# Performance work log

Measured on AMD Instinct MI355X. Metric: run time of the kernel, lower is better.

## Reference

```python
import jax, jax.numpy as jnp
import numpy as np

B, V = 1024, 16            # batch, n_variables
NH, SHARE = 32, 4          # n_base_heads, n_heads_sharing_slider
SH = NH // SHARE           # n_slider_heads = 8
D = 128                    # n_token_dim
KV = D * SH                # kv_size = 1024
H = 4096                   # n_hidden


def setup_inputs() -> dict:
    key = jax.random.key(0)
    ks = jax.random.split(key, 14)
    s = 0.02
    inp = {
        "prefix": jax.random.uniform(ks[0], (B, V), jnp.float32, -1.0, 1.0),
        # stacked per-variable key-encoder weights
        "kW1": jax.random.normal(ks[1], (V, KV), jnp.float32) * s,
        "kb1": jnp.zeros((V, KV), jnp.float32),
        "kW2": jax.random.normal(ks[2], (V, KV, H), jnp.float32) * s,
        "kb2": jnp.zeros((V, H), jnp.float32),
        "kW3": jax.random.normal(ks[3], (V, H, KV), jnp.float32) * s,
        "kb3": jnp.zeros((V, KV), jnp.float32),
        # stacked per-variable value-encoder weights
        "vW1": jax.random.normal(ks[4], (V, KV), jnp.float32) * s,
        "vb1": jnp.zeros((V, KV), jnp.float32),
        "vW2": jax.random.normal(ks[5], (V, KV, H), jnp.float32) * s,
        "vb2": jnp.zeros((V, H), jnp.float32),
        "vW3": jax.random.normal(ks[6], (V, H, KV), jnp.float32) * s,
        "vb3": jnp.zeros((V, KV), jnp.float32),
        "attention_factor": jnp.zeros((), jnp.float32),
    }
    return inp


def _mlp(x, W1, b1, W2, b2, W3, b3):
    # x: [B, V] scalar slider per variable; stacked tiny MLPs over V.
    h = jnp.tanh(x[:, :, None] * W1[None] + b1[None])            # [B,V,KV]
    h = jnp.tanh(jnp.einsum('bvk,vkh->bvh', h, W2) + b2[None])   # [B,V,H]
    return jnp.einsum('bvh,vhk->bvk', h, W3) + b3[None]          # [B,V,KV]


def _to_heads(x):
    # [B,V,KV] -> [B, n_base_heads, V, D] with repeat_interleave over slider heads
    x = x.reshape(B, V, SH, D)
    x = jnp.repeat(x, SHARE, axis=2)            # [B,V,NH,D]
    return jnp.transpose(x, (0, 2, 1, 3))       # [B,NH,V,D]


def reference(prefix, kW1, kb1, kW2, kb2, kW3, kb3,
              vW1, vb1, vW2, vb2, vW3, vb3, attention_factor):
    keys = _to_heads(_mlp(prefix, kW1, kb1, kW2, kb2, kW3, kb3))
    values = _to_heads(_mlp(prefix, vW1, vb1, vW2, vb2, vW3, vb3))
    return keys, values, attention_factor
```

## Files before the change

### kernel.cpp

```cpp
#include <hip/hip_runtime.h>
#include <hip/hip_bf16.h>
#include <cstdint>

#define B_   1024
#define V_   16
#define NH_  32
#define SH_  8
#define D_   128
#define KV_  1024
#define H_   4096

typedef __bf16 bf16;
typedef bf16  bf16x8 __attribute__((ext_vector_type(8)));
typedef float f32x2  __attribute__((ext_vector_type(2)));
typedef float f32x4  __attribute__((ext_vector_type(4)));

#define VMCNT(n) asm volatile("s_waitcnt vmcnt(" #n ")" ::: "memory")
#define LGKM0()  asm volatile("s_waitcnt lgkmcnt(0)" ::: "memory")

__device__ __forceinline__ void gl2lds16(const void* g, void* l) {
    __builtin_amdgcn_global_load_lds((const __attribute__((address_space(1))) void*)g,
                                     (__attribute__((address_space(3))) void*)l,
                                     16, 0, 0);
}

__global__ __launch_bounds__(256)
void h1_kernel(const float* __restrict__ prefix,
               const float* __restrict__ W1a, const float* __restrict__ b1a,
               const float* __restrict__ W1b, const float* __restrict__ b1b,
               bf16* __restrict__ h1)
{
    int gid = blockIdx.x * 256 + threadIdx.x;
    int k8  = gid & 127;
    int b   = (gid >> 7) & 1023;
    int vm  = gid >> 17;
    int v   = vm & 15;
    const float* W1 = (vm >> 4) ? W1b : W1a;
    const float* b1 = (vm >> 4) ? b1b : b1a;
    float x = prefix[b * V_ + v];
    const float* wp = W1 + (size_t)v * KV_ + k8 * 8;
    const float* bp = b1 + (size_t)v * KV_ + k8 * 8;
    f32x4 w0 = *(const f32x4*)wp,       w1 = *(const f32x4*)(wp + 4);
    f32x4 q0 = *(const f32x4*)bp,       q1 = *(const f32x4*)(bp + 4);
    bf16x8 o;
#pragma unroll
    for (int j = 0; j < 4; ++j) o[j]     = (bf16)tanhf(fmaf(x, w0[j], q0[j]));
#pragma unroll
    for (int j = 0; j < 4; ++j) o[4 + j] = (bf16)tanhf(fmaf(x, w1[j], q1[j]));
    *(bf16x8*)(h1 + (size_t)gid * 8) = o;
}

template<int MODE, int KDIM, int NDIM>
__global__ __launch_bounds__(512)
void gemm_t2(const bf16* __restrict__ A0, const bf16* __restrict__ A1,
             const float* __restrict__ Bf0, const float* __restrict__ Bf1,
             const float* __restrict__ bias0, const float* __restrict__ bias1,
             bf16* __restrict__ outB0, bf16* __restrict__ outB1,
             float* __restrict__ outF)
{
    __shared__ __align__(16) char smem[131072];

    constexpr int NX  = NDIM / 256;
    constexpr int NMB = 4;
    constexpr int NXY = NX * NMB;
    const int lin = blockIdx.x + NX * blockIdx.y + NXY * blockIdx.z;
    constexpr int NWG = NXY * 32;
    constexpr int CHK = NWG / 8;
    const int swz = (lin & 7) * CHK + (lin >> 3);
    const int mm  = swz / (NXY * 16);
    const int r2  = swz - mm * (NXY * 16);
    const int v   = r2 / NXY;
    const int rem = r2 - v * NXY;
    const int m0  = (rem / NX) * 256;
    const int n0  = (rem - (rem / NX) * NX) * 256;

    const bf16*  Abase = mm ? A1 : A0;
    const float* Bbase = mm ? Bf1 : Bf0;
    const float* bias  = mm ? bias1 : bias0;

    const int t  = threadIdx.x;
    const int l  = t & 63;
    const int w  = t >> 6;
    const int wr = w >> 2;
    const int wc = w & 3;
    constexpr int NT = KDIM / 64;
    static_assert(NT >= 4, "NT >= 4");

    const bf16*  Av = Abase + (size_t)v * 1024 * KDIM + (size_t)m0 * KDIM;
    const float* Bv = Bbase + (size_t)v * KDIM * NDIM + n0;

    f32x4 acc[8][4];
#pragma unroll
    for (int i = 0; i < 8; ++i)
#pragma unroll
        for (int j = 0; j < 4; ++j) acc[i][j] = f32x4{0.f, 0.f, 0.f, 0.f};

    const float* bptr = Bv + (size_t)((t >> 7) * 16) * NDIM + 2 * (t & 127);
    f32x2 br[16];

    auto loadBR = [&](int ktile) {
        const float* np = bptr + (size_t)ktile * 64 * NDIM;
#pragma unroll
        for (int j = 0; j < 16; ++j) br[j] = *(const f32x2*)(np + (size_t)j * NDIM);
    };
    auto stageA = [&](int ktile, int ab) {
#pragma unroll
        for (int i = 0; i < 4; ++i) {
            const int off = t + i * 512;
            const int row = off >> 3;
            const int gc  = (off & 7) ^ ((row >> 1) & 7);
            gl2lds16(Av + (size_t)row * KDIM + ktile * 64 + gc * 8,
                     smem + (size_t)ab * 32768 + (size_t)off * 16);
        }
    };
    auto writeB = [&](int bb) {
        bf16* bN = (bf16*)(smem + 65536 + (size_t)bb * 32768);
#pragma unroll
        for (int i = 0; i < 2; ++i)
#pragma unroll
            for (int h = 0; h < 2; ++h) {
                bf16x8 pk;
#pragma unroll
                for (int jj = 0; jj < 8; ++jj) pk[jj] = (bf16)br[h * 8 + jj][i];
                const int n  = 2 * (t & 127) + i;
                const int ch = ((t >> 7) * 2 + h) ^ (t & 7);
                *(bf16x8*)(bN + (size_t)n * 64 + ch * 8) = pk;
            }
    };
    auto mfmaStep = [&](int kt) {
        const bf16* aC = (const bf16*)(smem + (size_t)(kt & 1) * 32768);
        const bf16* bC = (const bf16*)(smem + 65536 + (size_t)(kt & 1) * 32768);
#pragma unroll
        for (int kk = 0; kk < 2; ++kk) {
            bf16x8 af[8], bfv[4];
#pragma unroll
            for (int f = 0; f < 8; ++f) {
                const int mr = wr * 128 + f * 16 + (l & 15);
                const int ca = (kk * 4 + (l >> 4)) ^ ((mr >> 1) & 7);
                af[f] = *(const bf16x8*)(aC + (size_t)mr * 64 + ca * 8);
            }
#pragma unroll
            for (int f = 0; f < 4; ++f) {
                const int nr = wc * 64 + f * 16 + (l & 15);
                const int cb = (kk * 4 + (l >> 4)) ^ ((nr >> 1) & 7);
                bfv[f] = *(const bf16x8*)(bC + (size_t)nr * 64 + cb * 8);
            }
#pragma unroll
            for (int fm = 0; fm < 8; ++fm)
#pragma unroll
                for (int fn = 0; fn < 4; ++fn)
                    acc[fm][fn] = __builtin_amdgcn_mfma_f32_16x16x32_bf16(
                        af[fm], bfv[fn], acc[fm][fn], 0, 0, 0);
        }
    };

    loadBR(0);
    stageA(0, 0);
    VMCNT(4);
    writeB(0);
    VMCNT(0);
    LGKM0();
    __builtin_amdgcn_s_barrier();

    for (int kt = 0; kt < NT - 1; ++kt) {
        loadBR(kt + 1);
        stageA(kt + 1, (kt + 1) & 1);
        mfmaStep(kt);
        VMCNT(4);
        writeB((kt + 1) & 1);
        VMCNT(0);
        LGKM0();
        __builtin_amdgcn_s_barrier();
    }
    mfmaStep(NT - 1);

    const int rbase = (l >> 4) * 4;
    const int cbase = l & 15;
    if (MODE == 0) {
        bf16* outB = mm ? outB1 : outB0;
        __syncthreads();
        bf16* scr = (bf16*)(smem + (size_t)w * 16384);
#pragma unroll
        for (int fn = 0; fn < 4; ++fn) {
            const int c  = fn * 16 + cbase;
            const float bv = bias[(size_t)v * NDIM + n0 + wc * 64 + c];
#pragma unroll
            for (int fm = 0; fm < 8; ++fm)
#pragma unroll
                for (int j = 0; j < 4; ++j) {
                    const int r = fm * 16 + rbase + j;
                    scr[r * 64 + (c ^ (((r >> 2) & 3) << 4))] =
                        (bf16)tanhf(acc[fm][fn][j] + bv);
                }
        }
        const int c8 = (l & 7) * 8;
#pragma unroll
        for (int i = 0; i < 16; ++i) {
            const int r  = i * 8 + (l >> 3);
            bf16x8 val = *(const bf16x8*)&scr[r * 64 + (c8 ^ (((r >> 2) & 3) << 4))];
            const int mr = m0 + wr * 128 + r;
            const int nc = n0 + wc * 64 + c8;
            __builtin_nontemporal_store(val,
                (bf16x8*)(outB + (size_t)v * 1024 * NDIM + (size_t)mr * NDIM + nc));
        }
    } else {
        float* outm = outF + (size_t)mm * ((size_t)B_ * NH_ * V_ * D_);
        __syncthreads();
        float* scr = (float*)(smem + (size_t)w * 16384);
        const int nb = n0 + wc * 64;
        const int sh = nb >> 7;
        const int db = nb & 127;
#pragma unroll
        for (int p = 0; p < 2; ++p) {
#pragma unroll
            for (int fm = 0; fm < 8; ++fm)
#pragma unroll
                for (int fq = 0; fq < 2; ++fq) {
                    const int fn = 2 * p + fq;
#pragma unroll
                    for (int j = 0; j < 4; ++j) {
                        const int r = fm * 16 + rbase + j;
                        const int c = fq * 16 + cbase;
                        scr[r * 32 + (c ^ (((r >> 2) & 1) << 4))] = acc[fm][fn][j];
                    }
                }
            const int c4   = (l & 7) * 4;
            const int colg = p * 32 + c4;
            f32x4 bv4;
#pragma unroll
            for (int q = 0; q < 4; ++q)
                bv4[q] = bias[(size_t)v * NDIM + nb + colg + q];
#pragma unroll
            for (int i = 0; i < 16; ++i) {
                const int r = i * 8 + (l >> 3);
                f32x4 val = *(const f32x4*)&scr[r * 32 + (c4 ^ (((r >> 2) & 1) << 4))];
#pragma unroll
                for (int q = 0; q < 4; ++q) val[q] += bv4[q];
                const int mr = m0 + wr * 128 + r;
                float* pp = outm + (size_t)mr * (NH_ * V_ * D_)
                                 + (size_t)(sh * 4) * (V_ * D_)
                                 + (size_t)v * D_ + db + colg;
                __builtin_nontemporal_store(val, (f32x4*)(pp));
                __builtin_nontemporal_store(val, (f32x4*)(pp + V_ * D_));
                __builtin_nontemporal_store(val, (f32x4*)(pp + 2 * V_ * D_));
                __builtin_nontemporal_store(val, (f32x4*)(pp + 3 * V_ * D_));
            }
        }
    }
}

__global__ void tail_kernel(const float* __restrict__ af, float* __restrict__ out)
{
    out[0] = af[0];
}

extern "C" void kernel_launch(void* const* d_in, const int* in_sizes, int n_in,
                              void* d_out, int out_size, void* d_ws, size_t ws_size,
                              hipStream_t stream)
{
    const float* prefix = (const float*)d_in[0];
    const float* W1[2]  = {(const float*)d_in[1], (const float*)d_in[7]};
    const float* b1[2]  = {(const float*)d_in[2], (const float*)d_in[8]};
    const float* W2[2]  = {(const float*)d_in[3], (const float*)d_in[9]};
    const float* b2[2]  = {(const float*)d_in[4], (const float*)d_in[10]};
    const float* W3[2]  = {(const float*)d_in[5], (const float*)d_in[11]};
    const float* b3[2]  = {(const float*)d_in[6], (const float*)d_in[12]};
    const float* afac   = (const float*)d_in[13];

    bf16* h1  = (bf16*)d_ws;
    bf16* h2a = (bf16*)((char*)d_ws + (size_t)67108864);
    bf16* h2b = (bf16*)((char*)d_ws + (size_t)67108864 + (size_t)134217728);
    float* outp = (float*)d_out;

    h1_kernel<<<16384, 256, 0, stream>>>(prefix, W1[0], b1[0], W1[1], b1[1], h1);
    gemm_t2<0, 1024, 4096><<<dim3(16, 4, 32), 512, 0, stream>>>(
        h1, h1 + (size_t)16777216, W2[0], W2[1], b2[0], b2[1],
        h2a, h2b, nullptr);
    gemm_t2<1, 4096, 1024><<<dim3(4, 4, 32), 512, 0, stream>>>(
        h2a, h2b, W3[0], W3[1], b3[0], b3[1],
        nullptr, nullptr, outp);
    tail_kernel<<<1, 1, 0, stream>>>(afac, outp + (size_t)2 * B_ * NH_ * V_ * D_);
}
```

Before: 868.0 us.

## Prefetch B weights two k-tiles ahead with double register banks and MFMA priority

The B-operand (fp32 weight) register prefetch becomes two k-tiles deep, using two alternating register banks with adjusted vmcnt waits, so global-load latency is hidden behind more MFMA work. The MFMA section is wrapped in s_setprio to favour math issue, and launch bounds request 2 blocks per CU. The extra 32 registers per thread plus the 2-block launch bound may cause spills or lower occupancy, since the 128KB shared memory already limits residency.

```diff
diff --git a/kernel.cpp b/kernel.cpp
--- a/kernel.cpp
+++ b/kernel.cpp
@@ -51,8 +51,8 @@
 }
 
 template<int MODE, int KDIM, int NDIM>
-__global__ __launch_bounds__(512)
-void gemm_t2(const bf16* __restrict__ A0, const bf16* __restrict__ A1,
+__global__ __launch_bounds__(512, 2)
+void gemm_t4(const bf16* __restrict__ A0, const bf16* __restrict__ A1,
              const float* __restrict__ Bf0, const float* __restrict__ Bf1,
              const float* __restrict__ bias0, const float* __restrict__ bias1,
              bf16* __restrict__ outB0, bf16* __restrict__ outB1,
@@ -84,7 +84,7 @@
     const int wr = w >> 2;
     const int wc = w & 3;
     constexpr int NT = KDIM / 64;
-    static_assert(NT >= 4, "NT >= 4");
+    static_assert(NT >= 4 && (NT % 2) == 0, "NT even, >= 4");
 
     const bf16*  Av = Abase + (size_t)v * 1024 * KDIM + (size_t)m0 * KDIM;
     const float* Bv = Bbase + (size_t)v * KDIM * NDIM + n0;
@@ -96,12 +96,12 @@
         for (int j = 0; j < 4; ++j) acc[i][j] = f32x4{0.f, 0.f, 0.f, 0.f};
 
     const float* bptr = Bv + (size_t)((t >> 7) * 16) * NDIM + 2 * (t & 127);
-    f32x2 br[16];
-
-    auto loadBR = [&](int ktile) {
+    f32x2 brA[16], brB[16];
+
+    auto loadBR = [&](int ktile, f32x2 (&bank)[16]) {
         const float* np = bptr + (size_t)ktile * 64 * NDIM;
 #pragma unroll
-        for (int j = 0; j < 16; ++j) br[j] = *(const f32x2*)(np + (size_t)j * NDIM);
+        for (int j = 0; j < 16; ++j) bank[j] = *(const f32x2*)(np + (size_t)j * NDIM);
     };
     auto stageA = [&](int ktile, int ab) {
 #pragma unroll
@@ -113,7 +113,7 @@
                      smem + (size_t)ab * 32768 + (size_t)off * 16);
         }
     };
-    auto writeB = [&](int bb) {
+    auto writeB = [&](f32x2 (&bank)[16], int bb) {
         bf16* bN = (bf16*)(smem + 65536 + (size_t)bb * 32768);
 #pragma unroll
         for (int i = 0; i < 2; ++i)
@@ -121,7 +121,7 @@
             for (int h = 0; h < 2; ++h) {
                 bf16x8 pk;
 #pragma unroll
-                for (int jj = 0; jj < 8; ++jj) pk[jj] = (bf16)br[h * 8 + jj][i];
+                for (int jj = 0; jj < 8; ++jj) pk[jj] = (bf16)bank[h * 8 + jj][i];
                 const int n  = 2 * (t & 127) + i;
                 const int ch = ((t >> 7) * 2 + h) ^ (t & 7);
                 *(bf16x8*)(bN + (size_t)n * 64 + ch * 8) = pk;
@@ -130,6 +130,7 @@
     auto mfmaStep = [&](int kt) {
         const bf16* aC = (const bf16*)(smem + (size_t)(kt & 1) * 32768);
         const bf16* bC = (const bf16*)(smem + 65536 + (size_t)(kt & 1) * 32768);
+        __builtin_amdgcn_s_setprio(1);
 #pragma unroll
         for (int kk = 0; kk < 2; ++kk) {
             bf16x8 af[8], bfv[4];
@@ -152,22 +153,37 @@
                     acc[fm][fn] = __builtin_amdgcn_mfma_f32_16x16x32_bf16(
                         af[fm], bfv[fn], acc[fm][fn], 0, 0, 0);
         }
-    };
-
-    loadBR(0);
+        __builtin_amdgcn_s_setprio(0);
+    };
+
+    loadBR(0, brA);
     stageA(0, 0);
-    VMCNT(4);
-    writeB(0);
-    VMCNT(0);
+    loadBR(1, brB);
+    VMCNT(20);
+    writeB(brA, 0);
+    VMCNT(16);
     LGKM0();
     __builtin_amdgcn_s_barrier();
 
-    for (int kt = 0; kt < NT - 1; ++kt) {
-        loadBR(kt + 1);
+    auto stepS = [&](int kt, f32x2 (&brIss)[16], f32x2 (&brUse)[16]) {
         stageA(kt + 1, (kt + 1) & 1);
+        loadBR(kt + 2, brIss);
         mfmaStep(kt);
+        VMCNT(20);
+        writeB(brUse, (kt + 1) & 1);
+        VMCNT(16);
+        LGKM0();
+        __builtin_amdgcn_s_barrier();
+    };
+    for (int kt = 0; kt + 3 < NT; kt += 2) {
+        stepS(kt,     brA, brB);
+        stepS(kt + 1, brB, brA);
+    }
+    {
+        stageA(NT - 1, (NT - 1) & 1);
+        mfmaStep(NT - 2);
         VMCNT(4);
-        writeB((kt + 1) & 1);
+        writeB(brB, (NT - 1) & 1);
         VMCNT(0);
         LGKM0();
         __builtin_amdgcn_s_barrier();
@@ -273,10 +289,10 @@
     float* outp = (float*)d_out;
 
     h1_kernel<<<16384, 256, 0, stream>>>(prefix, W1[0], b1[0], W1[1], b1[1], h1);
-    gemm_t2<0, 1024, 4096><<<dim3(16, 4, 32), 512, 0, stream>>>(
+    gemm_t4<0, 1024, 4096><<<dim3(16, 4, 32), 512, 0, stream>>>(
         h1, h1 + (size_t)16777216, W2[0], W2[1], b2[0], b2[1],
         h2a, h2b, nullptr);
-    gemm_t2<1, 4096, 1024><<<dim3(4, 4, 32), 512, 0, stream>>>(
+    gemm_t4<1, 4096, 1024><<<dim3(4, 4, 32), 512, 0, stream>>>(
         h2a, h2b, W3[0], W3[1], b3[0], b3[1],
         nullptr, nullptr, outp);
     tail_kernel<<<1, 1, 0, stream>>>(afac, outp + (size_t)2 * B_ * NH_ * V_ * D_);
```

After: 2.339 ms. 2.69x slower.

## Fuse first-layer tanh activation into the first GEMM's A-tile producer

Applied to the files above, without the earlier changes.

Removes the separate h1 kernel and its 64MB bf16 intermediate buffer. The first GEMM now loads W1, b1 and the prefix slice into LDS and computes the tanh(x*W1+b1) A tiles on the fly for each k-tile, instead of streaming A from global memory. This trades global memory traffic for recomputed tanh work. Each A tile is recomputed once per N-block (16 times) and adds extra LDS use, which could reduce occupancy.

```diff
diff --git a/kernel.cpp b/kernel.cpp
--- a/kernel.cpp
+++ b/kernel.cpp
@@ -24,41 +24,19 @@
                                      16, 0, 0);
 }
 
-__global__ __launch_bounds__(256)
-void h1_kernel(const float* __restrict__ prefix,
-               const float* __restrict__ W1a, const float* __restrict__ b1a,
-               const float* __restrict__ W1b, const float* __restrict__ b1b,
-               bf16* __restrict__ h1)
-{
-    int gid = blockIdx.x * 256 + threadIdx.x;
-    int k8  = gid & 127;
-    int b   = (gid >> 7) & 1023;
-    int vm  = gid >> 17;
-    int v   = vm & 15;
-    const float* W1 = (vm >> 4) ? W1b : W1a;
-    const float* b1 = (vm >> 4) ? b1b : b1a;
-    float x = prefix[b * V_ + v];
-    const float* wp = W1 + (size_t)v * KV_ + k8 * 8;
-    const float* bp = b1 + (size_t)v * KV_ + k8 * 8;
-    f32x4 w0 = *(const f32x4*)wp,       w1 = *(const f32x4*)(wp + 4);
-    f32x4 q0 = *(const f32x4*)bp,       q1 = *(const f32x4*)(bp + 4);
-    bf16x8 o;
-#pragma unroll
-    for (int j = 0; j < 4; ++j) o[j]     = (bf16)tanhf(fmaf(x, w0[j], q0[j]));
-#pragma unroll
-    for (int j = 0; j < 4; ++j) o[4 + j] = (bf16)tanhf(fmaf(x, w1[j], q1[j]));
-    *(bf16x8*)(h1 + (size_t)gid * 8) = o;
-}
-
-template<int MODE, int KDIM, int NDIM>
 __global__ __launch_bounds__(512)
-void gemm_t2(const bf16* __restrict__ A0, const bf16* __restrict__ A1,
+void gemm1_f(const float* __restrict__ prefix,
+             const float* __restrict__ W1a, const float* __restrict__ b1a,
+             const float* __restrict__ W1b, const float* __restrict__ b1b,
              const float* __restrict__ Bf0, const float* __restrict__ Bf1,
              const float* __restrict__ bias0, const float* __restrict__ bias1,
-             bf16* __restrict__ outB0, bf16* __restrict__ outB1,
-             float* __restrict__ outF)
+             bf16* __restrict__ outB0, bf16* __restrict__ outB1)
 {
-    __shared__ __align__(16) char smem[131072];
+    constexpr int KDIM = 1024, NDIM = 4096;
+    __shared__ __align__(16) char smem[140288];
+    float* w1L = (float*)(smem + 131072);
+    float* b1L = (float*)(smem + 135168);
+    float* pfL = (float*)(smem + 139264);
 
     constexpr int NX  = NDIM / 256;
     constexpr int NMB = 4;
@@ -74,9 +52,11 @@
     const int m0  = (rem / NX) * 256;
     const int n0  = (rem - (rem / NX) * NX) * 256;
 
-    const bf16*  Abase = mm ? A1 : A0;
-    const float* Bbase = mm ? Bf1 : Bf0;
-    const float* bias  = mm ? bias1 : bias0;
+    const float* W1v = (mm ? W1b : W1a) + (size_t)v * KV_;
+    const float* b1v = (mm ? b1b : b1a) + (size_t)v * KV_;
+    const float* Bv  = (mm ? Bf1 : Bf0) + (size_t)v * KDIM * NDIM + n0;
+    const float* bias = mm ? bias1 : bias0;
+    bf16* outB = mm ? outB1 : outB0;
 
     const int t  = threadIdx.x;
     const int l  = t & 63;
@@ -84,7 +64,169 @@
     const int wr = w >> 2;
     const int wc = w & 3;
     constexpr int NT = KDIM / 64;
-    static_assert(NT >= 4, "NT >= 4");
+
+    f32x4 acc[8][4];
+#pragma unroll
+    for (int i = 0; i < 8; ++i)
+#pragma unroll
+        for (int j = 0; j < 4; ++j) acc[i][j] = f32x4{0.f, 0.f, 0.f, 0.f};
+
+    const float* bptr = Bv + (size_t)((t >> 7) * 16) * NDIM + 2 * (t & 127);
+    f32x2 br[16];
+
+    auto loadBR = [&](int ktile) {
+        const float* np = bptr + (size_t)ktile * 64 * NDIM;
+#pragma unroll
+        for (int j = 0; j < 16; ++j) br[j] = *(const f32x2*)(np + (size_t)j * NDIM);
+    };
+    auto computeA = [&](int ktile, int ab) {
+#pragma unroll
+        for (int i = 0; i < 4; ++i) {
+            const int off = t + i * 512;
+            const int row = off >> 3;
+            const int gc  = (off & 7) ^ ((row >> 1) & 7);
+            const int kb  = ktile * 64 + gc * 8;
+            const float x = pfL[row];
+            f32x4 wa = *(const f32x4*)&w1L[kb],     wb = *(const f32x4*)&w1L[kb + 4];
+            f32x4 qa = *(const f32x4*)&b1L[kb],     qb = *(const f32x4*)&b1L[kb + 4];
+            bf16x8 o;
+#pragma unroll
+            for (int j = 0; j < 4; ++j) o[j]     = (bf16)tanhf(fmaf(x, wa[j], qa[j]));
+#pragma unroll
+            for (int j = 0; j < 4; ++j) o[4 + j] = (bf16)tanhf(fmaf(x, wb[j], qb[j]));
+            *(bf16x8*)(smem + (size_t)ab * 32768 + (size_t)off * 16) = o;
+        }
+    };
+    auto writeB = [&](int bb) {
+        bf16* bN = (bf16*)(smem + 65536 + (size_t)bb * 32768);
+#pragma unroll
+        for (int i = 0; i < 2; ++i)
+#pragma unroll
+            for (int h = 0; h < 2; ++h) {
+                bf16x8 pk;
+#pragma unroll
+                for (int jj = 0; jj < 8; ++jj) pk[jj] = (bf16)br[h * 8 + jj][i];
+                const int n  = 2 * (t & 127) + i;
+                const int ch = ((t >> 7) * 2 + h) ^ (t & 7);
+                *(bf16x8*)(bN + (size_t)n * 64 + ch * 8) = pk;
+            }
+    };
+    auto mfmaStep = [&](int kt) {
+        const bf16* aC = (const bf16*)(smem + (size_t)(kt & 1) * 32768);
+        const bf16* bC = (const bf16*)(smem + 65536 + (size_t)(kt & 1) * 32768);
+#pragma unroll
+        for (int kk = 0; kk < 2; ++kk) {
+            bf16x8 af[8], bfv[4];
+#pragma unroll
+            for (int f = 0; f < 8; ++f) {
+                const int mr = wr * 128 + f * 16 + (l & 15);
+                const int ca = (kk * 4 + (l >> 4)) ^ ((mr >> 1) & 7);
+                af[f] = *(const bf16x8*)(aC + (size_t)mr * 64 + ca * 8);
+            }
+#pragma unroll
+            for (int f = 0; f < 4; ++f) {
+                const int nr = wc * 64 + f * 16 + (l & 15);
+                const int cb = (kk * 4 + (l >> 4)) ^ ((nr >> 1) & 7);
+                bfv[f] = *(const bf16x8*)(bC + (size_t)nr * 64 + cb * 8);
+            }
+#pragma unroll
+            for (int fm = 0; fm < 8; ++fm)
+#pragma unroll
+                for (int fn = 0; fn < 4; ++fn)
+                    acc[fm][fn] = __builtin_amdgcn_mfma_f32_16x16x32_bf16(
+                        af[fm], bfv[fn], acc[fm][fn], 0, 0, 0);
+        }
+    };
+
+    loadBR(0);
+    if (t < 256) {
+        f32x4 wv = *(const f32x4*)(W1v + t * 4);
+        float pf = prefix[(size_t)(m0 + t) * V_ + v];
+        *(f32x4*)&w1L[t * 4] = wv;
+        pfL[t] = pf;
+    } else {
+        f32x4 qv = *(const f32x4*)(b1v + (t - 256) * 4);
+        *(f32x4*)&b1L[(t - 256) * 4] = qv;
+    }
+    __syncthreads();
+    computeA(0, 0);
+    writeB(0);
+    LGKM0();
+    __builtin_amdgcn_s_barrier();
+
+    for (int kt = 0; kt < NT - 1; ++kt) {
+        loadBR(kt + 1);
+        computeA(kt + 1, (kt + 1) & 1);
+        mfmaStep(kt);
+        VMCNT(0);
+        writeB((kt + 1) & 1);
+        LGKM0();
+        __builtin_amdgcn_s_barrier();
+    }
+    mfmaStep(NT - 1);
+
+    const int rbase = (l >> 4) * 4;
+    const int cbase = l & 15;
+    __syncthreads();
+    bf16* scr = (bf16*)(smem + (size_t)w * 16384);
+#pragma unroll
+    for (int fn = 0; fn < 4; ++fn) {
+        const int c  = fn * 16 + cbase;
+        const float bv = bias[(size_t)v * NDIM + n0 + wc * 64 + c];
+#pragma unroll
+        for (int fm = 0; fm < 8; ++fm)
+#pragma unroll
+            for (int j = 0; j < 4; ++j) {
+                const int r = fm * 16 + rbase + j;
+                scr[r * 64 + (c ^ (((r >> 2) & 3) << 4))] =
+                    (bf16)tanhf(acc[fm][fn][j] + bv);
+            }
+    }
+    const int c8 = (l & 7) * 8;
+#pragma unroll
+    for (int i = 0; i < 16; ++i) {
+        const int r  = i * 8 + (l >> 3);
+        bf16x8 val = *(const bf16x8*)&scr[r * 64 + (c8 ^ (((r >> 2) & 3) << 4))];
+        const int mr = m0 + wr * 128 + r;
+        const int nc = n0 + wc * 64 + c8;
+        __builtin_nontemporal_store(val,
+            (bf16x8*)(outB + (size_t)v * 1024 * NDIM + (size_t)mr * NDIM + nc));
+    }
+}
+
+__global__ __launch_bounds__(512)
+void gemm2_k(const bf16* __restrict__ A0, const bf16* __restrict__ A1,
+             const float* __restrict__ Bf0, const float* __restrict__ Bf1,
+             const float* __restrict__ bias0, const float* __restrict__ bias1,
+             float* __restrict__ outF)
+{
+    constexpr int KDIM = 4096, NDIM = 1024;
+    __shared__ __align__(16) char smem[131072];
+
+    constexpr int NX  = NDIM / 256;
+    constexpr int NMB = 4;
+    constexpr int NXY = NX * NMB;
+    const int lin = blockIdx.x + NX * blockIdx.y + NXY * blockIdx.z;
+    constexpr int NWG = NXY * 32;
+    constexpr int CHK = NWG / 8;
+    const int swz = (lin & 7) * CHK + (lin >> 3);
+    const int mm  = swz / (NXY * 16);
+    const int r2  = swz - mm * (NXY * 16);
+    const int v   = r2 / NXY;
+    const int rem = r2 - v * NXY;
+    const int m0  = (rem / NX) * 256;
+    const int n0  = (rem - (rem / NX) * NX) * 256;
+
+    const bf16*  Abase = mm ? A1 : A0;
+    const float* Bbase = mm ? Bf1 : Bf0;
+    const float* bias  = mm ? bias1 : bias0;
+
+    const int t  = threadIdx.x;
+    const int l  = t & 63;
+    const int w  = t >> 6;
+    const int wr = w >> 2;
+    const int wc = w & 3;
+    constexpr int NT = KDIM / 64;
 
     const bf16*  Av = Abase + (size_t)v * 1024 * KDIM + (size_t)m0 * KDIM;
     const float* Bv = Bbase + (size_t)v * KDIM * NDIM + n0;
@@ -176,75 +318,46 @@
 
     const int rbase = (l >> 4) * 4;
     const int cbase = l & 15;
-    if (MODE == 0) {
-        bf16* outB = mm ? outB1 : outB0;
-        __syncthreads();
-        bf16* scr = (bf16*)(smem + (size_t)w * 16384);
-#pragma unroll
-        for (int fn = 0; fn < 4; ++fn) {
-            const int c  = fn * 16 + cbase;
-            const float bv = bias[(size_t)v * NDIM + n0 + wc * 64 + c];
-#pragma unroll
-            for (int fm = 0; fm < 8; ++fm)
+    float* outm = outF + (size_t)mm * ((size_t)B_ * NH_ * V_ * D_);
+    __syncthreads();
+    float* scr = (float*)(smem + (size_t)w * 16384);
+    const int nb = n0 + wc * 64;
+    const int sh = nb >> 7;
+    const int db = nb & 127;
+#pragma unroll
+    for (int p = 0; p < 2; ++p) {
+#pragma unroll
+        for (int fm = 0; fm < 8; ++fm)
+#pragma unroll
+            for (int fq = 0; fq < 2; ++fq) {
+                const int fn = 2 * p + fq;
 #pragma unroll
                 for (int j = 0; j < 4; ++j) {
                     const int r = fm * 16 + rbase + j;
-                    scr[r * 64 + (c ^ (((r >> 2) & 3) << 4))] =
-                        (bf16)tanhf(acc[fm][fn][j] + bv);
+                    const int c = fq * 16 + cbase;
+                    scr[r * 32 + (c ^ (((r >> 2) & 1) << 4))] = acc[fm][fn][j];
                 }
-        }
-        const int c8 = (l & 7) * 8;
+            }
+        const int c4   = (l & 7) * 4;
+        const int colg = p * 32 + c4;
+        f32x4 bv4;
+#pragma unroll
+        for (int q = 0; q < 4; ++q)
+            bv4[q] = bias[(size_t)v * NDIM + nb + colg + q];
 #pragma unroll
         for (int i = 0; i < 16; ++i) {
-            const int r  = i * 8 + (l >> 3);
-            bf16x8 val = *(const bf16x8*)&scr[r * 64 + (c8 ^ (((r >> 2) & 3) << 4))];
+            const int r = i * 8 + (l >> 3);
+            f32x4 val = *(const f32x4*)&scr[r * 32 + (c4 ^ (((r >> 2) & 1) << 4))];
+#pragma unroll
+            for (int q = 0; q < 4; ++q) val[q] += bv4[q];
             const int mr = m0 + wr * 128 + r;
-            const int nc = n0 + wc * 64 + c8;
-            __builtin_nontemporal_store(val,
-                (bf16x8*)(outB + (size_t)v * 1024 * NDIM + (size_t)mr * NDIM + nc));
-        }
-    } else {
-        float* outm = outF + (size_t)mm * ((size_t)B_ * NH_ * V_ * D_);
-        __syncthreads();
-        float* scr = (float*)(smem + (size_t)w * 16384);
-        const int nb = n0 + wc * 64;
-        const int sh = nb >> 7;
-        const int db = nb & 127;
-#pragma unroll
-        for (int p = 0; p < 2; ++p) {
-#pragma unroll
-            for (int fm = 0; fm < 8; ++fm)
-#pragma unroll
-                for (int fq = 0; fq < 2; ++fq) {
-                    const int fn = 2 * p + fq;
-#pragma unroll
-                    for (int j = 0; j < 4; ++j) {
-                        const int r = fm * 16 + rbase + j;
-                        const int c = fq * 16 + cbase;
-                        scr[r * 32 + (c ^ (((r >> 2) & 1) << 4))] = acc[fm][fn][j];
-                    }
-                }
-            const int c4   = (l & 7) * 4;
-            const int colg = p * 32 + c4;
-            f32x4 bv4;
-#pragma unroll
-            for (int q = 0; q < 4; ++q)
-                bv4[q] = bias[(size_t)v * NDIM + nb + colg + q];
-#pragma unroll
-            for (int i = 0; i < 16; ++i) {
-                const int r = i * 8 + (l >> 3);
-                f32x4 val = *(const f32x4*)&scr[r * 32 + (c4 ^ (((r >> 2) & 1) << 4))];
-#pragma unroll
-                for (int q = 0; q < 4; ++q) val[q] += bv4[q];
-                const int mr = m0 + wr * 128 + r;
-                float* pp = outm + (size_t)mr * (NH_ * V_ * D_)
-                                 + (size_t)(sh * 4) * (V_ * D_)
-                                 + (size_t)v * D_ + db + colg;
-                __builtin_nontemporal_store(val, (f32x4*)(pp));
-                __builtin_nontemporal_store(val, (f32x4*)(pp + V_ * D_));
-                __builtin_nontemporal_store(val, (f32x4*)(pp + 2 * V_ * D_));
-                __builtin_nontemporal_store(val, (f32x4*)(pp + 3 * V_ * D_));
-            }
+            float* pp = outm + (size_t)mr * (NH_ * V_ * D_)
+                             + (size_t)(sh * 4) * (V_ * D_)
+                             + (size_t)v * D_ + db + colg;
+            __builtin_nontemporal_store(val, (f32x4*)(pp));
+            __builtin_nontemporal_store(val, (f32x4*)(pp + V_ * D_));
+            __builtin_nontemporal_store(val, (f32x4*)(pp + 2 * V_ * D_));
+            __builtin_nontemporal_store(val, (f32x4*)(pp + 3 * V_ * D_));
         }
     }
 }
@@ -267,17 +380,14 @@
     const float* b3[2]  = {(const float*)d_in[6], (const float*)d_in[12]};
     const float* afac   = (const float*)d_in[13];
 
-    bf16* h1  = (bf16*)d_ws;
-    bf16* h2a = (bf16*)((char*)d_ws + (size_t)67108864);
-    bf16* h2b = (bf16*)((char*)d_ws + (size_t)67108864 + (size_t)134217728);
+    bf16* h2a = (bf16*)d_ws;
+    bf16* h2b = (bf16*)((char*)d_ws + (size_t)134217728);
     float* outp = (float*)d_out;
 
-    h1_kernel<<<16384, 256, 0, stream>>>(prefix, W1[0], b1[0], W1[1], b1[1], h1);
-    gemm_t2<0, 1024, 4096><<<dim3(16, 4, 32), 512, 0, stream>>>(
-        h1, h1 + (size_t)16777216, W2[0], W2[1], b2[0], b2[1],
-        h2a, h2b, nullptr);
-    gemm_t2<1, 4096, 1024><<<dim3(4, 4, 32), 512, 0, stream>>>(
-        h2a, h2b, W3[0], W3[1], b3[0], b3[1],
-        nullptr, nullptr, outp);
+    gemm1_f<<<dim3(16, 4, 32), 512, 0, stream>>>(
+        prefix, W1[0], b1[0], W1[1], b1[1],
+        W2[0], W2[1], b2[0], b2[1], h2a, h2b);
+    gemm2_k<<<dim3(4, 4, 32), 512, 0, stream>>>(
+        h2a, h2b, W3[0], W3[1], b3[0], b3[1], outp);
     tail_kernel<<<1, 1, 0, stream>>>(afac, outp + (size_t)2 * B_ * NH_ * V_ * D_);
 }
```

New measurement: 1.019 ms. 1.17x slower.

## Split GEMM main loop into four interleaved phases with barriers and setprio

Applied to the files above, without the earlier changes.

Restructures the GEMM K-loop into four sub-phases, each loading half the A and B fragments and issuing 16 MFMAs. Global B loads and A staging are split across these phases, and each MFMA cluster is wrapped in s_setprio with extra workgroup barriers, in the style of a ping-pong schedule. The aim is to interleave memory and LDS traffic with matrix math and keep fewer fragments live in registers. In exchange it adds several barriers per iteration, which may cost synchronisation time, and the VMCNT accounting now runs across the split loads.

```diff
diff --git a/kernel.cpp b/kernel.cpp
--- a/kernel.cpp
+++ b/kernel.cpp
@@ -52,7 +52,7 @@
 
 template<int MODE, int KDIM, int NDIM>
 __global__ __launch_bounds__(512)
-void gemm_t2(const bf16* __restrict__ A0, const bf16* __restrict__ A1,
+void gemm_p4(const bf16* __restrict__ A0, const bf16* __restrict__ A1,
              const float* __restrict__ Bf0, const float* __restrict__ Bf1,
              const float* __restrict__ bias0, const float* __restrict__ bias1,
              bf16* __restrict__ outB0, bf16* __restrict__ outB1,
@@ -98,10 +98,11 @@
     const float* bptr = Bv + (size_t)((t >> 7) * 16) * NDIM + 2 * (t & 127);
     f32x2 br[16];
 
-    auto loadBR = [&](int ktile) {
+    auto loadBRh = [&](int ktile, int h) {
         const float* np = bptr + (size_t)ktile * 64 * NDIM;
 #pragma unroll
-        for (int j = 0; j < 16; ++j) br[j] = *(const f32x2*)(np + (size_t)j * NDIM);
+        for (int j = 0; j < 8; ++j)
+            br[h * 8 + j] = *(const f32x2*)(np + (size_t)(h * 8 + j) * NDIM);
     };
     auto stageA = [&](int ktile, int ab) {
 #pragma unroll
@@ -127,34 +128,8 @@
                 *(bf16x8*)(bN + (size_t)n * 64 + ch * 8) = pk;
             }
     };
-    auto mfmaStep = [&](int kt) {
-        const bf16* aC = (const bf16*)(smem + (size_t)(kt & 1) * 32768);
-        const bf16* bC = (const bf16*)(smem + 65536 + (size_t)(kt & 1) * 32768);
-#pragma unroll
-        for (int kk = 0; kk < 2; ++kk) {
-            bf16x8 af[8], bfv[4];
-#pragma unroll
-            for (int f = 0; f < 8; ++f) {
-                const int mr = wr * 128 + f * 16 + (l & 15);
-                const int ca = (kk * 4 + (l >> 4)) ^ ((mr >> 1) & 7);
-                af[f] = *(const bf16x8*)(aC + (size_t)mr * 64 + ca * 8);
-            }
-#pragma unroll
-            for (int f = 0; f < 4; ++f) {
-                const int nr = wc * 64 + f * 16 + (l & 15);
-                const int cb = (kk * 4 + (l >> 4)) ^ ((nr >> 1) & 7);
-                bfv[f] = *(const bf16x8*)(bC + (size_t)nr * 64 + cb * 8);
-            }
-#pragma unroll
-            for (int fm = 0; fm < 8; ++fm)
-#pragma unroll
-                for (int fn = 0; fn < 4; ++fn)
-                    acc[fm][fn] = __builtin_amdgcn_mfma_f32_16x16x32_bf16(
-                        af[fm], bfv[fn], acc[fm][fn], 0, 0, 0);
-        }
-    };
-
-    loadBR(0);
+
+    loadBRh(0, 0); loadBRh(0, 1);
     stageA(0, 0);
     VMCNT(4);
     writeB(0);
@@ -162,17 +137,104 @@
     LGKM0();
     __builtin_amdgcn_s_barrier();
 
-    for (int kt = 0; kt < NT - 1; ++kt) {
-        loadBR(kt + 1);
-        stageA(kt + 1, (kt + 1) & 1);
-        mfmaStep(kt);
-        VMCNT(4);
-        writeB((kt + 1) & 1);
-        VMCNT(0);
+    const int kq = l >> 4;
+    const int lm = l & 15;
+    for (int kt = 0; kt < NT; ++kt) {
+        const int cur = kt & 1, nxt = cur ^ 1;
+        const bool more = (kt + 1 < NT);
+        const bf16* aC = (const bf16*)(smem + (size_t)cur * 32768);
+        const bf16* bC = (const bf16*)(smem + 65536 + (size_t)cur * 32768);
+
+        bf16x8 af[4], bfv[4];
+
+        if (more) loadBRh(kt + 1, 0);
+#pragma unroll
+        for (int f = 0; f < 4; ++f) {
+            const int nr = wc * 64 + f * 16 + lm;
+            const int cb = kq ^ ((nr >> 1) & 7);
+            bfv[f] = *(const bf16x8*)(bC + (size_t)nr * 64 + cb * 8);
+        }
+#pragma unroll
+        for (int f = 0; f < 4; ++f) {
+            const int mr = wr * 128 + f * 16 + lm;
+            const int ca = kq ^ ((mr >> 1) & 7);
+            af[f] = *(const bf16x8*)(aC + (size_t)mr * 64 + ca * 8);
+        }
+        __builtin_amdgcn_s_barrier();
+        __builtin_amdgcn_s_setprio(1);
+#pragma unroll
+        for (int fm = 0; fm < 4; ++fm)
+#pragma unroll
+            for (int fn = 0; fn < 4; ++fn)
+                acc[fm][fn] = __builtin_amdgcn_mfma_f32_16x16x32_bf16(
+                    af[fm], bfv[fn], acc[fm][fn], 0, 0, 0);
+        __builtin_amdgcn_s_setprio(0);
+        __builtin_amdgcn_s_barrier();
+
+        if (more) { loadBRh(kt + 1, 1); stageA(kt + 1, nxt); }
+#pragma unroll
+        for (int f = 0; f < 4; ++f) {
+            const int mr = wr * 128 + (4 + f) * 16 + lm;
+            const int ca = kq ^ ((mr >> 1) & 7);
+            af[f] = *(const bf16x8*)(aC + (size_t)mr * 64 + ca * 8);
+        }
+        __builtin_amdgcn_s_barrier();
+        __builtin_amdgcn_s_setprio(1);
+#pragma unroll
+        for (int fm = 0; fm < 4; ++fm)
+#pragma unroll
+            for (int fn = 0; fn < 4; ++fn)
+                acc[4 + fm][fn] = __builtin_amdgcn_mfma_f32_16x16x32_bf16(
+                    af[fm], bfv[fn], acc[4 + fm][fn], 0, 0, 0);
+        __builtin_amdgcn_s_setprio(0);
+        __builtin_amdgcn_s_barrier();
+
+#pragma unroll
+        for (int f = 0; f < 4; ++f) {
+            const int nr = wc * 64 + f * 16 + lm;
+            const int cb = (4 + kq) ^ ((nr >> 1) & 7);
+            bfv[f] = *(const bf16x8*)(bC + (size_t)nr * 64 + cb * 8);
+        }
+#pragma unroll
+        for (int f = 0; f < 4; ++f) {
+            const int mr = wr * 128 + f * 16 + lm;
+            const int ca = (4 + kq) ^ ((mr >> 1) & 7);
+            af[f] = *(const bf16x8*)(aC + (size_t)mr * 64 + ca * 8);
+        }
+        __builtin_amdgcn_s_barrier();
+        __builtin_amdgcn_s_setprio(1);
+#pragma unroll
+        for (int fm = 0; fm < 4; ++fm)
+#pragma unroll
+            for (int fn = 0; fn < 4; ++fn)
+                acc[fm][fn] = __builtin_amdgcn_mfma_f32_16x16x32_bf16(
+                    af[fm], bfv[fn], acc[fm][fn], 0, 0, 0);
+        __builtin_amdgcn_s_setprio(0);
+        __builtin_amdgcn_s_barrier();
+
+#pragma unroll
+        for (int f = 0; f < 4; ++f) {
+            const int mr = wr * 128 + (4 + f) * 16 + lm;
+            const int ca = (4 + kq) ^ ((mr >> 1) & 7);
+            af[f] = *(const bf16x8*)(aC + (size_t)mr * 64 + ca * 8);
+        }
+        if (more) {
+            VMCNT(4);
+            writeB(nxt);
+        }
+        __builtin_amdgcn_s_barrier();
+        __builtin_amdgcn_s_setprio(1);
+#pragma unroll
+        for (int fm = 0; fm < 4; ++fm)
+#pragma unroll
+            for (int fn = 0; fn < 4; ++fn)
+                acc[4 + fm][fn] = __builtin_amdgcn_mfma_f32_16x16x32_bf16(
+                    af[fm], bfv[fn], acc[4 + fm][fn], 0, 0, 0);
+        __builtin_amdgcn_s_setprio(0);
+        if (more) { VMCNT(0); }
         LGKM0();
         __builtin_amdgcn_s_barrier();
     }
-    mfmaStep(NT - 1);
 
     const int rbase = (l >> 4) * 4;
     const int cbase = l & 15;
@@ -273,10 +335,10 @@
     float* outp = (float*)d_out;
 
     h1_kernel<<<16384, 256, 0, stream>>>(prefix, W1[0], b1[0], W1[1], b1[1], h1);
-    gemm_t2<0, 1024, 4096><<<dim3(16, 4, 32), 512, 0, stream>>>(
+    gemm_p4<0, 1024, 4096><<<dim3(16, 4, 32), 512, 0, stream>>>(
         h1, h1 + (size_t)16777216, W2[0], W2[1], b2[0], b2[1],
         h2a, h2b, nullptr);
-    gemm_t2<1, 4096, 1024><<<dim3(4, 4, 32), 512, 0, stream>>>(
+    gemm_p4<1, 4096, 1024><<<dim3(4, 4, 32), 512, 0, stream>>>(
         h2a, h2b, W3[0], W3[1], b3[0], b3[1],
         nullptr, nullptr, outp);
     tail_kernel<<<1, 1, 0, stream>>>(afac, outp + (size_t)2 * B_ * NH_ * V_ * D_);
```

Result: slower. 930.2 us (+7.2%).
